# Performance work log

Measured on AMD Instinct MI355X. Metric: run time of the kernel, lower is better.

## Reference

```python
import jax, jax.numpy as jnp
import numpy as np

K = 3        # kernel_size
S = 1        # stride
P = 1        # padding
SCALE = 1000.0  # scale_factor
SUMMARY = 'avg'


def _unfold(x, k, s, p):
    # torch.nn.functional.unfold: (N,C,H,W) -> (N, C*k*k, L), channel-major then (kh,kw)
    N, C, H, W = x.shape
    Hout = (H + 2 * p - k) // s + 1
    Wout = (W + 2 * p - k) // s + 1
    xp = jnp.pad(x, ((0, 0), (0, 0), (p, p), (p, p)))
    cols = [xp[:, :, ki:ki + s * Hout:s, kj:kj + s * Wout:s]
            for ki in range(k) for kj in range(k)]
    patches = jnp.stack(cols, axis=2)  # (N, C, k*k, Hout, Wout)
    return patches.reshape(N, C * k * k, Hout * Wout), Hout, Wout


def _rep_first(s):
    # For each position l, index of the FIRST position j with s[j] == s[l].
    # Equivalent to unique(return_index, return_inverse): ui[di[l]].
    L = s.shape[0]
    order = jnp.argsort(s)                 # stable sort (jax default)
    ss = s[order]
    is_new = jnp.concatenate([jnp.ones((1,), bool), ss[1:] != ss[:-1]])
    pos = jnp.where(is_new, jnp.arange(L), 0)
    last_new = jax.lax.cummax(pos)         # position (in sorted order) of current group start
    rep_sorted = order[last_new]           # first-occurrence original index per group
    return jnp.zeros(L, jnp.int32).at[order].set(rep_sorted.astype(jnp.int32))


def setup_inputs() -> dict:
    key = jax.random.key(0)
    k1, k2, k3 = jax.random.split(key, 3)
    fmap = jax.random.normal(k1, (8, 64, 128, 128), dtype=jnp.float32)
    weight = jax.random.normal(k2, (128, 576), dtype=jnp.float32) * 0.05
    bias = jax.random.normal(k3, (128, 1), dtype=jnp.float32) * 0.05
    return {"fmap": fmap, "weight": weight, "bias": bias}


def reference(fmap, weight, bias):
    cols, Hout, Wout = _unfold(fmap, K, S, P)          # (N, Cin*K*K, L)
    if SUMMARY == 'avg':
        summ = cols.mean(axis=1)                        # (N, L)
    else:
        summ = cols.max(axis=1)
    summ = (summ * SCALE).astype(jnp.int32)             # trunc toward zero, like .int()
    rep = jax.vmap(_rep_first)(summ)                    # (N, L) representative patch index
    gathered = jnp.take_along_axis(cols, rep[:, None, :], axis=2)  # (N, P, L)
    out = jnp.einsum('op,npl->nol', weight, gathered) + bias[None]  # (N, Cout, L)
    N = fmap.shape[0]
    return out.reshape(N, weight.shape[0], Hout, Wout)
```

## Files before the change

kernel.cpp:

```cpp
#include <hip/hip_runtime.h>
#include <stdint.h>

#define NIMG 8
#define CIN 64
#define HH 128
#define WWID 128
#define L (HH*WWID)
#define COUT 128
#define PATCH 576
#define TBL 4096
#define OFFV 2048
#define CAP 4096
#define SPB 8
#define POISON 0xAAAAAAAAu

__global__ __launch_bounds__(256) void csq_kernel(const float* __restrict__ fmap,
                                                  const float* __restrict__ W,
                                                  float* __restrict__ Wt,
                                                  int* __restrict__ qarr,
                                                  unsigned int* __restrict__ firstIdx) {
    int bid  = blockIdx.x;
    int n    = bid >> 5;
    int tile = bid & 31;
    int h0   = tile << 2;
    int tid  = threadIdx.x;

    {
        int base = bid * 288;
        for (int i = tid; i < 288; i += 256) {
            int idx = base + i;
            int k = idx >> 7, o = idx & 127;
            Wt[idx] = W[o * PATCH + k];
        }
    }

    __shared__ double cs[6 * 128];
    const float* fb = fmap + (size_t)n * CIN * L;

    if (tid < 192) {
        int r  = tid / 32;
        int wg = (tid & 31) << 2;
        int h  = h0 + r - 1;
        double s0 = 0, s1 = 0, s2 = 0, s3 = 0;
        if (h >= 0 && h < HH) {
            const float* q = fb + h * WWID + wg;
            #pragma unroll 8
            for (int c = 0; c < CIN; ++c) {
                float4 v = *(const float4*)(q + (size_t)c * L);
                s0 += (double)v.x; s1 += (double)v.y; s2 += (double)v.z; s3 += (double)v.w;
            }
        }
        double* d = cs + r * 128 + wg;
        d[0] = s0; d[1] = s1; d[2] = s2; d[3] = s3;
    }
    __syncthreads();

    #pragma unroll
    for (int po = tid; po < 4 * 128; po += 256) {
        int oh = po >> 7, ow = po & 127;
        double s = 0.0;
        #pragma unroll
        for (int ki = 0; ki < 3; ++ki) {
            const double* row = cs + (oh + ki) * 128;
            #pragma unroll
            for (int kj = 0; kj < 3; ++kj) {
                int w = ow + kj - 1;
                if ((unsigned)w < 128u) s += row[w];
            }
        }
        double avg = s / 576.0;
        int q = (int)(avg * 1000.0);
        int hw = (h0 + oh) * WWID + ow;
        qarr[n * L + hw] = q;
        int v = q + OFFV;
        v = v < 0 ? 0 : (v > TBL - 1 ? TBL - 1 : v);
        atomicMin(&firstIdx[(size_t)n * TBL + v], (unsigned int)hw);
    }
}

__global__ void compact_kernel(const unsigned int* __restrict__ firstIdx,
                               int* __restrict__ slotTab, unsigned int* __restrict__ uniqJ,
                               unsigned int* __restrict__ count) {
    int idx = blockIdx.x * blockDim.x + threadIdx.x;
    if (idx >= NIMG * TBL) return;
    unsigned int fi = firstIdx[idx];
    if (fi < 0x10000u) {
        int n = idx >> 12;
        unsigned int s = atomicAdd(&count[n], 1u) - POISON;
        slotTab[idx] = (int)s;
        if (s < CAP) uniqJ[n * CAP + s] = fi;
    }
}

__global__ __launch_bounds__(256) void gemm_kernel(const float* __restrict__ fmap,
                            const float* __restrict__ Wt, const float* __restrict__ bias,
                            const unsigned int* __restrict__ uniqJ,
                            const unsigned int* __restrict__ count,
                            float* __restrict__ R) {
    int bid = blockIdx.x;
    int n   = bid & 7;
    int s0  = (bid >> 3) * SPB;
    unsigned int cntu = count[n] - POISON;
    int cnt = cntu > CAP ? CAP : (int)cntu;
    if (s0 >= cnt) return;

    __shared__ float patch[SPB][PATCH];
    __shared__ float part[3][64][2][SPB];
    int tid = threadIdx.x;

    #pragma unroll
    for (int i = tid; i < SPB * PATCH; i += 256) {
        int si = i / PATCH, p = i - si * PATCH;
        float v = 0.f;
        int s = s0 + si;
        if (s < cnt) {
            unsigned int j = uniqJ[n * CAP + s];
            int hj = j >> 7, wj = j & 127;
            int c = p / 9, r = p - c * 9;
            int hh = hj + r / 3 - 1;
            int ww = wj + (r % 3) - 1;
            if (hh >= 0 && hh < HH && ww >= 0 && ww < WWID)
                v = fmap[((size_t)n * CIN + c) * L + hh * WWID + ww];
        }
        patch[si][p] = v;
    }
    __syncthreads();

    int op = tid & 63;
    int kq = tid >> 6;
    int kbase = kq * (PATCH / 4);

    float acc[2][SPB];
    #pragma unroll
    for (int j = 0; j < 2; ++j)
        #pragma unroll
        for (int i = 0; i < SPB; ++i) acc[j][i] = 0.f;

    const float* wp = Wt + (size_t)kbase * COUT + op * 2;
    #pragma unroll 2
    for (int kk = 0; kk < PATCH / 4; kk += 4) {
        float2 w0 = *(const float2*)(wp + (kk + 0) * COUT);
        float2 w1 = *(const float2*)(wp + (kk + 1) * COUT);
        float2 w2 = *(const float2*)(wp + (kk + 2) * COUT);
        float2 w3 = *(const float2*)(wp + (kk + 3) * COUT);
        #pragma unroll
        for (int i = 0; i < SPB; ++i) {
            float4 pv = *(const float4*)(&patch[i][kbase + kk]);
            acc[0][i] += w0.x * pv.x + w1.x * pv.y + w2.x * pv.z + w3.x * pv.w;
            acc[1][i] += w0.y * pv.x + w1.y * pv.y + w2.y * pv.z + w3.y * pv.w;
        }
    }

    if (kq) {
        #pragma unroll
        for (int j = 0; j < 2; ++j)
            #pragma unroll
            for (int i = 0; i < SPB; ++i) part[kq - 1][op][j][i] = acc[j][i];
    }
    __syncthreads();
    if (kq == 0) {
        #pragma unroll
        for (int j = 0; j < 2; ++j) {
            int o = op * 2 + j;
            float b = bias[o];
            float* Rrow = R + ((size_t)n * COUT + o) * CAP;
            #pragma unroll
            for (int i = 0; i < SPB; ++i) {
                int s = s0 + i;
                if (s < cnt)
                    Rrow[s] = acc[j][i] + part[0][op][j][i] + part[1][op][j][i]
                            + part[2][op][j][i] + b;
            }
        }
    }
}

__global__ __launch_bounds__(256) void scatter_kernel(const float* __restrict__ weight,
                               const float* __restrict__ bias, const float* __restrict__ fmap,
                               const int* __restrict__ qarr, const int* __restrict__ slotTab,
                               const unsigned int* __restrict__ firstIdx,
                               const float* __restrict__ R, float* __restrict__ out) {
    int idx = blockIdx.x * blockDim.x + threadIdx.x;
    if (idx >= NIMG * COUT * L / 4) return;
    int l4 = (idx & (L / 4 - 1)) << 2;
    int o  = (idx >> 12) & 127;
    int n  = idx >> 19;

    int4 q4 = *(const int4*)(qarr + (size_t)n * L + l4);
    const int* st = slotTab + (size_t)n * TBL;
    const float* Rrow = R + ((size_t)n * COUT + o) * CAP;

    float4 val;
    float* vp = (float*)&val;
    const int* qp = (const int*)&q4;
    #pragma unroll
    for (int e = 0; e < 4; ++e) {
        int q = qp[e];
        int v = q + OFFV;
        v = v < 0 ? 0 : (v > TBL - 1 ? TBL - 1 : v);
        int s = st[v];
        if (s < CAP) {
            vp[e] = Rrow[s];
        } else {
            unsigned int j = firstIdx[(size_t)n * TBL + v];
            int h0 = j >> 7, w0 = j & 127;
            const float* wr = weight + (size_t)o * PATCH;
            float acc = 0.f;
            for (int c = 0; c < CIN; ++c)
                for (int r = 0; r < 9; ++r) {
                    int hh = h0 + r / 3 - 1;
                    int ww = w0 + (r % 3) - 1;
                    float pv = (hh >= 0 && hh < HH && ww >= 0 && ww < WWID)
                               ? fmap[((size_t)n * CIN + c) * L + hh * WWID + ww] : 0.f;
                    acc += wr[c * 9 + r] * pv;
                }
            vp[e] = acc + bias[o];
        }
    }
    *(float4*)(out + ((size_t)n * COUT + o) * L + l4) = val;
}

extern "C" void kernel_launch(void* const* d_in, const int* in_sizes, int n_in,
                              void* d_out, int out_size, void* d_ws, size_t ws_size,
                              hipStream_t stream) {
    const float* fmap   = (const float*)d_in[0];
    const float* weight = (const float*)d_in[1];
    const float* bias   = (const float*)d_in[2];
    float* out = (float*)d_out;

    char* ws = (char*)d_ws;
    int*          qarr     = (int*)ws;           ws += (size_t)NIMG * L * 4;
    unsigned int* firstIdx = (unsigned int*)ws;  ws += (size_t)NIMG * TBL * 4;
    int*          slotTab  = (int*)ws;           ws += (size_t)NIMG * TBL * 4;
    unsigned int* uniqJ    = (unsigned int*)ws;  ws += (size_t)NIMG * CAP * 4;
    unsigned int* count    = (unsigned int*)ws;  ws += 128;
    float*        Wt       = (float*)ws;         ws += (size_t)COUT * PATCH * 4;
    float*        R        = (float*)ws;         ws += (size_t)NIMG * COUT * CAP * 4;

    csq_kernel<<<NIMG * 32, 256, 0, stream>>>(fmap, weight, Wt, qarr, firstIdx);
    compact_kernel<<<(NIMG * TBL + 255) / 256, 256, 0, stream>>>(firstIdx, slotTab, uniqJ, count);
    int gblocks = (CAP / SPB) * NIMG;
    gemm_kernel<<<gblocks, 256, 0, stream>>>(fmap, Wt, bias, uniqJ, count, R);
    int no4 = NIMG * COUT * L / 4;
    scatter_kernel<<<(no4 + 255) / 256, 256, 0, stream>>>(weight, bias, fmap, qarr, slotTab, firstIdx, R, out);
}
```

Baseline: 186.2 us.

## Fuse four kernels into one cooperative persistent kernel with grid syncs

Replaces the four separate launches (quantize/first-index, compact, gemm, scatter) with a single cooperative kernel of 512 blocks that runs each stage as a phase separated by grid.sync(). The gemm and scatter stages become grid-stride loops over the same work, and shared memory is unioned across phases. This targets per-launch overhead and inter-kernel gaps. In exchange, the stages have less parallelism than the original launches provided and each phase pays a grid barrier. The original kernels remain as a fallback if cooperative launch is unavailable.

Measured after the change: 339.3 us. 82.3% more time.

```diff
diff --git a/kernel.cpp b/kernel.cpp
--- a/kernel.cpp
+++ b/kernel.cpp
@@ -1,5 +1,8 @@
 #include <hip/hip_runtime.h>
+#include <hip/hip_cooperative_groups.h>
 #include <stdint.h>
+
+namespace cg = cooperative_groups;
 
 #define NIMG 8
 #define CIN 64
@@ -13,30 +16,14 @@
 #define CAP 4096
 #define SPB 8
 #define POISON 0xAAAAAAAAu
-
-__global__ __launch_bounds__(256) void csq_kernel(const float* __restrict__ fmap,
-                                                  const float* __restrict__ W,
-                                                  float* __restrict__ Wt,
-                                                  int* __restrict__ qarr,
-                                                  unsigned int* __restrict__ firstIdx) {
-    int bid  = blockIdx.x;
-    int n    = bid >> 5;
-    int tile = bid & 31;
-    int h0   = tile << 2;
-    int tid  = threadIdx.x;
-
-    {
-        int base = bid * 288;
-        for (int i = tid; i < 288; i += 256) {
-            int idx = base + i;
-            int k = idx >> 7, o = idx & 127;
-            Wt[idx] = W[o * PATCH + k];
-        }
-    }
-
-    __shared__ double cs[6 * 128];
+#define GRID 512
+
+
+__device__ __forceinline__ void csq_phase(int cb, int tid, const float* __restrict__ fmap,
+        int* __restrict__ qarr, unsigned int* __restrict__ firstIdx, double* cs) {
+    int n = cb >> 5, tile = cb & 31;
+    int h0 = tile << 2;
     const float* fb = fmap + (size_t)n * CIN * L;
-
     if (tid < 192) {
         int r  = tid / 32;
         int wg = (tid & 31) << 2;
@@ -54,7 +41,6 @@
         d[0] = s0; d[1] = s1; d[2] = s2; d[3] = s3;
     }
     __syncthreads();
-
     #pragma unroll
     for (int po = tid; po < 4 * 128; po += 256) {
         int oh = po >> 7, ow = po & 127;
@@ -78,11 +64,9 @@
     }
 }
 
-__global__ void compact_kernel(const unsigned int* __restrict__ firstIdx,
-                               int* __restrict__ slotTab, unsigned int* __restrict__ uniqJ,
-                               unsigned int* __restrict__ count) {
-    int idx = blockIdx.x * blockDim.x + threadIdx.x;
-    if (idx >= NIMG * TBL) return;
+__device__ __forceinline__ void compact_phase(int idx, const unsigned int* __restrict__ firstIdx,
+        int* __restrict__ slotTab, unsigned int* __restrict__ uniqJ,
+        unsigned int* __restrict__ count) {
     unsigned int fi = firstIdx[idx];
     if (fi < 0x10000u) {
         int n = idx >> 12;
@@ -92,21 +76,15 @@
     }
 }
 
-__global__ __launch_bounds__(256) void gemm_kernel(const float* __restrict__ fmap,
-                            const float* __restrict__ Wt, const float* __restrict__ bias,
-                            const unsigned int* __restrict__ uniqJ,
-                            const unsigned int* __restrict__ count,
-                            float* __restrict__ R) {
-    int bid = blockIdx.x;
-    int n   = bid & 7;
-    int s0  = (bid >> 3) * SPB;
+__device__ __forceinline__ void gemm_phase(int vb, int tid, const float* __restrict__ fmap,
+        const float* __restrict__ Wt, const float* __restrict__ bias,
+        const unsigned int* __restrict__ uniqJ, const unsigned int* __restrict__ count,
+        float* __restrict__ R, float* patch , float* part ) {
+    int n  = vb & 7;
+    int s0 = (vb >> 3) * SPB;
     unsigned int cntu = count[n] - POISON;
     int cnt = cntu > CAP ? CAP : (int)cntu;
     if (s0 >= cnt) return;
-
-    __shared__ float patch[SPB][PATCH];
-    __shared__ float part[3][64][2][SPB];
-    int tid = threadIdx.x;
 
     #pragma unroll
     for (int i = tid; i < SPB * PATCH; i += 256) {
@@ -122,7 +100,7 @@
             if (hh >= 0 && hh < HH && ww >= 0 && ww < WWID)
                 v = fmap[((size_t)n * CIN + c) * L + hh * WWID + ww];
         }
-        patch[si][p] = v;
+        patch[si * PATCH + p] = v;
     }
     __syncthreads();
 
@@ -145,17 +123,18 @@
         float2 w3 = *(const float2*)(wp + (kk + 3) * COUT);
         #pragma unroll
         for (int i = 0; i < SPB; ++i) {
-            float4 pv = *(const float4*)(&patch[i][kbase + kk]);
+            float4 pv = *(const float4*)(patch + i * PATCH + kbase + kk);
             acc[0][i] += w0.x * pv.x + w1.x * pv.y + w2.x * pv.z + w3.x * pv.w;
             acc[1][i] += w0.y * pv.x + w1.y * pv.y + w2.y * pv.z + w3.y * pv.w;
         }
     }
 
     if (kq) {
+        float* pb = part + ((kq - 1) * 64 + op) * 2 * SPB;
         #pragma unroll
         for (int j = 0; j < 2; ++j)
             #pragma unroll
-            for (int i = 0; i < SPB; ++i) part[kq - 1][op][j][i] = acc[j][i];
+            for (int i = 0; i < SPB; ++i) pb[j * SPB + i] = acc[j][i];
     }
     __syncthreads();
     if (kq == 0) {
@@ -164,24 +143,23 @@
             int o = op * 2 + j;
             float b = bias[o];
             float* Rrow = R + ((size_t)n * COUT + o) * CAP;
+            const float* p0 = part + (0 * 64 + op) * 2 * SPB + j * SPB;
+            const float* p1 = part + (1 * 64 + op) * 2 * SPB + j * SPB;
+            const float* p2 = part + (2 * 64 + op) * 2 * SPB + j * SPB;
             #pragma unroll
             for (int i = 0; i < SPB; ++i) {
                 int s = s0 + i;
-                if (s < cnt)
-                    Rrow[s] = acc[j][i] + part[0][op][j][i] + part[1][op][j][i]
-                            + part[2][op][j][i] + b;
+                if (s < cnt) Rrow[s] = acc[j][i] + p0[i] + p1[i] + p2[i] + b;
             }
         }
     }
 }
 
-__global__ __launch_bounds__(256) void scatter_kernel(const float* __restrict__ weight,
-                               const float* __restrict__ bias, const float* __restrict__ fmap,
-                               const int* __restrict__ qarr, const int* __restrict__ slotTab,
-                               const unsigned int* __restrict__ firstIdx,
-                               const float* __restrict__ R, float* __restrict__ out) {
-    int idx = blockIdx.x * blockDim.x + threadIdx.x;
-    if (idx >= NIMG * COUT * L / 4) return;
+__device__ __forceinline__ void scatter_phase(int idx, const float* __restrict__ weight,
+        const float* __restrict__ bias, const float* __restrict__ fmap,
+        const int* __restrict__ qarr, const int* __restrict__ slotTab,
+        const unsigned int* __restrict__ firstIdx, const float* __restrict__ R,
+        float* __restrict__ out) {
     int l4 = (idx & (L / 4 - 1)) << 2;
     int o  = (idx >> 12) & 127;
     int n  = idx >> 19;
@@ -195,8 +173,7 @@
     const int* qp = (const int*)&q4;
     #pragma unroll
     for (int e = 0; e < 4; ++e) {
-        int q = qp[e];
-        int v = q + OFFV;
+        int v = qp[e] + OFFV;
         v = v < 0 ? 0 : (v > TBL - 1 ? TBL - 1 : v);
         int s = st[v];
         if (s < CAP) {
@@ -220,6 +197,83 @@
     *(float4*)(out + ((size_t)n * COUT + o) * L + l4) = val;
 }
 
+__global__ __launch_bounds__(256) void fused_kernel(const float* __restrict__ fmap,
+        const float* __restrict__ W, const float* __restrict__ bias,
+        float* __restrict__ Wt, int* __restrict__ qarr, unsigned int* __restrict__ firstIdx,
+        int* __restrict__ slotTab, unsigned int* __restrict__ uniqJ,
+        unsigned int* __restrict__ count, float* __restrict__ R, float* __restrict__ out) {
+    cg::grid_group grid = cg::this_grid();
+    __shared__ __align__(16) char sm[SPB * PATCH * 4 + 3 * 64 * 2 * SPB * 4];
+    double* cs   = (double*)sm;
+    float* patch = (float*)sm;
+    float* part  = (float*)(sm + SPB * PATCH * 4);
+    int bid = blockIdx.x, tid = threadIdx.x;
+
+    {
+        int base = bid * 144;
+        for (int i = tid; i < 144; i += 256) {
+            int idx = base + i;
+            int k = idx >> 7, o = idx & 127;
+            Wt[idx] = W[o * PATCH + k];
+        }
+    }
+    if (bid < NIMG * 32) csq_phase(bid, tid, fmap, qarr, firstIdx, cs);
+    grid.sync();
+
+    {
+        int idx = bid * 256 + tid;
+        if (idx < NIMG * TBL) compact_phase(idx, firstIdx, slotTab, uniqJ, count);
+    }
+    grid.sync();
+
+    for (int vb = bid; vb < (CAP / SPB) * NIMG; vb += GRID)
+        gemm_phase(vb, tid, fmap, Wt, bias, uniqJ, count, R, patch, part);
+    grid.sync();
+
+    for (int idx = bid * 256 + tid; idx < NIMG * COUT * L / 4; idx += GRID * 256)
+        scatter_phase(idx, W, bias, fmap, qarr, slotTab, firstIdx, R, out);
+}
+
+__global__ __launch_bounds__(256) void csq_kernel(const float* __restrict__ fmap,
+        const float* __restrict__ W, float* __restrict__ Wt,
+        int* __restrict__ qarr, unsigned int* __restrict__ firstIdx) {
+    __shared__ double cs[6 * 128];
+    int bid = blockIdx.x, tid = threadIdx.x;
+    int base = bid * 288;
+    for (int i = tid; i < 288; i += 256) {
+        int idx = base + i;
+        int k = idx >> 7, o = idx & 127;
+        Wt[idx] = W[o * PATCH + k];
+    }
+    csq_phase(bid, tid, fmap, qarr, firstIdx, cs);
+}
+
+__global__ void compact_kernel(const unsigned int* __restrict__ firstIdx,
+        int* __restrict__ slotTab, unsigned int* __restrict__ uniqJ,
+        unsigned int* __restrict__ count) {
+    int idx = blockIdx.x * blockDim.x + threadIdx.x;
+    if (idx < NIMG * TBL) compact_phase(idx, firstIdx, slotTab, uniqJ, count);
+}
+
+__global__ __launch_bounds__(256) void gemm_kernel(const float* __restrict__ fmap,
+        const float* __restrict__ Wt, const float* __restrict__ bias,
+        const unsigned int* __restrict__ uniqJ, const unsigned int* __restrict__ count,
+        float* __restrict__ R) {
+    __shared__ __align__(16) float patch[SPB * PATCH];
+    __shared__ float part[3 * 64 * 2 * SPB];
+    gemm_phase(blockIdx.x, threadIdx.x, fmap, Wt, bias, uniqJ, count, R, patch, part);
+}
+
+__global__ __launch_bounds__(256) void scatter_kernel(const float* __restrict__ weight,
+        const float* __restrict__ bias, const float* __restrict__ fmap,
+        const int* __restrict__ qarr, const int* __restrict__ slotTab,
+        const unsigned int* __restrict__ firstIdx, const float* __restrict__ R,
+        float* __restrict__ out) {
+    int idx = blockIdx.x * blockDim.x + threadIdx.x;
+    if (idx < NIMG * COUT * L / 4)
+        scatter_phase(idx, weight, bias, fmap, qarr, slotTab, firstIdx, R, out);
+}
+
 extern "C" void kernel_launch(void* const* d_in, const int* in_sizes, int n_in,
                               void* d_out, int out_size, void* d_ws, size_t ws_size,
                               hipStream_t stream) {
@@ -237,10 +291,30 @@
     float*        Wt       = (float*)ws;         ws += (size_t)COUT * PATCH * 4;
     float*        R        = (float*)ws;         ws += (size_t)NIMG * COUT * CAP * 4;
 
-    csq_kernel<<<NIMG * 32, 256, 0, stream>>>(fmap, weight, Wt, qarr, firstIdx);
-    compact_kernel<<<(NIMG * TBL + 255) / 256, 256, 0, stream>>>(firstIdx, slotTab, uniqJ, count);
-    int gblocks = (CAP / SPB) * NIMG;
-    gemm_kernel<<<gblocks, 256, 0, stream>>>(fmap, Wt, bias, uniqJ, count, R);
-    int no4 = NIMG * COUT * L / 4;
-    scatter_kernel<<<(no4 + 255) / 256, 256, 0, stream>>>(weight, bias, fmap, qarr, slotTab, firstIdx, R, out);
-}
+    static int coop_ok = -1;
+    if (coop_ok < 0) {
+        int dev = 0; hipGetDevice(&dev);
+        int has_coop = 0, ncu = 0, nb = 0;
+        hipDeviceGetAttribute(&has_coop, hipDeviceAttributeCooperativeLaunch, dev);
+        hipDeviceGetAttribute(&ncu, hipDeviceAttributeMultiprocessorCount, dev);
+        hipOccupancyMaxActiveBlocksPerMultiprocessor(&nb, fused_kernel, 256, 0);
+        coop_ok = (has_coop && (long)nb * ncu >= GRID) ? 1 : 0;
+    }
+
+    bool launched = false;
+    if (coop_ok == 1) {
+        void* args[] = {(void*)&fmap, (void*)&weight, (void*)&bias, (void*)&Wt,
+                        (void*)&qarr, (void*)&firstIdx, (void*)&slotTab, (void*)&uniqJ,
+                        (void*)&count, (void*)&R, (void*)&out};
+        hipError_t e = hipLaunchCooperativeKernel((const void*)fused_kernel,
+                                                  dim3(GRID), dim3(256), args, 0, stream);
+        launched = (e == hipSuccess);
+    }
+    if (!launched) {
+        csq_kernel<<<NIMG * 32, 256, 0, stream>>>(fmap, weight, Wt, qarr, firstIdx);
+        compact_kernel<<<(NIMG * TBL + 255) / 256, 256, 0, stream>>>(firstIdx, slotTab, uniqJ, count);
+        gemm_kernel<<<(CAP / SPB) * NIMG, 256, 0, stream>>>(fmap, Wt, bias, uniqJ, count, R);
+        scatter_kernel<<<(NIMG * COUT * L / 4 + 255) / 256, 256, 0, stream>>>(
+            weight, bias, fmap, qarr, slotTab, firstIdx, R, out);
+    }
+}
```
